# Kernel tuning notes

Measured on AMD Instinct MI355X. Metric: run time of the kernel, lower is better.

## Reference

```python
import jax, jax.numpy as jnp
import numpy as np


def rotary_pos_emb(x):
    # x: [..., seq, dim], dim even. Interleaved (GPT-NeoX-style pairwise) rotary.
    dim, seq = x.shape[-1], x.shape[-2]
    ts = jnp.arange(0, dim, 2, dtype=jnp.float32)
    inv_freqs = 10000.0 ** (-ts / dim)
    grid = jnp.arange(seq, dtype=jnp.float32)[:, None] * inv_freqs[None, :]  # [s, dim//2]
    sin = jnp.repeat(jnp.sin(grid), 2, axis=-1).astype(x.dtype)  # [s, dim]
    cos = jnp.repeat(jnp.cos(grid), 2, axis=-1).astype(x.dtype)  # [s, dim]
    x1, x2 = x[..., ::2], x[..., 1::2]
    xs = jnp.stack([-x2, x1], axis=-1).reshape(x.shape)  # interleave (-x2, x1)
    return x * cos + xs * sin


def setup_inputs() -> dict:
    key = jax.random.key(0)
    kx, kq, kk, kv, ko = jax.random.split(key, 5)
    B, S, D = 2, 2048, 1024
    scale = 1.0 / np.sqrt(D)
    x = jax.random.normal(kx, (B, S, D), dtype=jnp.float32)
    mask = jnp.tril(jnp.ones((S, S), dtype=bool))  # causal
    Wq = jax.random.normal(kq, (D, D), dtype=jnp.float32) * scale
    Wk = jax.random.normal(kk, (D, D), dtype=jnp.float32) * scale
    Wv = jax.random.normal(kv, (D, D), dtype=jnp.float32) * scale
    Wo = jax.random.normal(ko, (D, D), dtype=jnp.float32) * scale
    return {"x": x, "mask": mask, "Wq": Wq, "Wk": Wk, "Wv": Wv, "Wo": Wo}


def reference(x, mask, Wq, Wk, Wv, Wo):
    H = 16
    POS_PORTION = 0.5
    B, S, D = x.shape
    K = D // H
    p = int(K * POS_PORTION)

    q = (x @ Wq) / (K ** 0.5)
    q = q.reshape(B, S, H, K).transpose(0, 2, 1, 3)  # b h l k
    q = jnp.concatenate([rotary_pos_emb(q[..., :p]), q[..., p:]], axis=-1)

    k = (x @ Wk).reshape(B, S, H, K).transpose(0, 2, 1, 3)
    k = jnp.concatenate([rotary_pos_emb(k[..., :p]), k[..., p:]], axis=-1)

    v = (x @ Wv).reshape(B, S, H, K).transpose(0, 2, 1, 3)

    logits = jnp.einsum('bhik,bhjk->bhij', q, k)
    # full-precision masked softmax
    l32 = logits.astype(jnp.float32)
    l32 = jnp.where(mask, l32, -1e30)
    a = jax.nn.softmax(l32, axis=-1).astype(logits.dtype)

    y = jnp.einsum('bhij,bhjv->bhiv', a, v)
    y = y.transpose(0, 2, 1, 3).reshape(B, S, D)  # b l (h v)
    return y @ Wo
```

## Files before the change

### kernel.cpp

```cpp
#include <hip/hip_runtime.h>
#include <cstdint>
#include <cstddef>

typedef __bf16 bf16;
typedef __bf16 bf16x8 __attribute__((ext_vector_type(8)));
typedef float  f32x4  __attribute__((ext_vector_type(4)));
typedef short  s16x4  __attribute__((ext_vector_type(4)));

#define B_  2
#define S_  2048
#define D_  1024
#define H_  16
#define KH  64

__device__ __forceinline__ void gload_lds16(const bf16* gp, bf16* lds_base) {
    __builtin_amdgcn_global_load_lds(
        (const __attribute__((address_space(1))) unsigned int*)gp,
        (__attribute__((address_space(3))) unsigned int*)lds_base,
        16, 0, 0);
}

__global__ __launch_bounds__(256) void prep(
    const float* __restrict__ x, bf16* __restrict__ xb,
    const float* __restrict__ Wq, const float* __restrict__ Wk,
    const float* __restrict__ Wv, const float* __restrict__ Wo,
    bf16* __restrict__ WqkvT, bf16* __restrict__ WoT)
{
    __shared__ bf16 tl[64][72];
    int z = blockIdx.x;
    if (z < 4096) {
        const int i = (z * 256 + threadIdx.x) * 4;
        const float4 v = *(const float4*)(x + i);
        union { int2 w; bf16 e[4]; } u;
        u.e[0] = (bf16)v.x; u.e[1] = (bf16)v.y;
        u.e[2] = (bf16)v.z; u.e[3] = (bf16)v.w;
        *(int2*)(xb + i) = u.w;
        return;
    }
    z -= 4096;
    const int zx = z & 15, zy = (z >> 4) & 15, zw = z >> 8;
    const float* src = (zw == 0) ? Wq : (zw == 1) ? Wk : (zw == 2) ? Wv : Wo;
    bf16* dst = (zw < 3) ? (WqkvT + (size_t)zw * D_ * D_) : WoT;
    const int r0 = zy * 64;
    const int c0 = zx * 64;
    const int t  = threadIdx.x;
    {
        const int r = t >> 2, cs = (t & 3) * 16;
        const float4* p = (const float4*)(src + (size_t)(r0 + r) * D_ + c0 + cs);
        float4 a0 = p[0], a1 = p[1], a2 = p[2], a3 = p[3];
        tl[cs +  0][r] = (bf16)a0.x; tl[cs +  1][r] = (bf16)a0.y;
        tl[cs +  2][r] = (bf16)a0.z; tl[cs +  3][r] = (bf16)a0.w;
        tl[cs +  4][r] = (bf16)a1.x; tl[cs +  5][r] = (bf16)a1.y;
        tl[cs +  6][r] = (bf16)a1.z; tl[cs +  7][r] = (bf16)a1.w;
        tl[cs +  8][r] = (bf16)a2.x; tl[cs +  9][r] = (bf16)a2.y;
        tl[cs + 10][r] = (bf16)a2.z; tl[cs + 11][r] = (bf16)a2.w;
        tl[cs + 12][r] = (bf16)a3.x; tl[cs + 13][r] = (bf16)a3.y;
        tl[cs + 14][r] = (bf16)a3.z; tl[cs + 15][r] = (bf16)a3.w;
    }
    __syncthreads();
    {
        const int c = t >> 2, rs = (t & 3) * 16;
        union { int4 v[2]; bf16 e[16]; } u;
#pragma unroll
        for (int i = 0; i < 16; ++i) u.e[i] = tl[c][rs + i];
        int4* p = (int4*)(dst + (size_t)(c0 + c) * D_ + r0 + rs);
        p[0] = u.v[0]; p[1] = u.v[1];
    }
}

template <int EPI, int BN>
__global__ __launch_bounds__(256, 2) void gemm_bt(
    const bf16* __restrict__ A, const bf16* __restrict__ BT,
    float* __restrict__ C, int N, int Kd,
    bf16* __restrict__ qp, bf16* __restrict__ kp, bf16* __restrict__ vp)
{
    constexpr int NJF = BN / 32;
    __shared__ bf16 As[128 * 64];
    __shared__ bf16 Bs[BN * 64];
    const int tid  = threadIdx.x;
    const int lane = tid & 63;
    const int wave = tid >> 6;
    const int l15  = lane & 15;
    const int quad = lane >> 4;
    const int m0 = blockIdx.y * 128;
    const int n0 = blockIdx.x * BN;
    const int wm = (wave >> 1) * 64;
    const int wn = (wave & 1) * (BN / 2);

    f32x4 acc[4][NJF];
#pragma unroll
    for (int i = 0; i < 4; ++i)
#pragma unroll
        for (int j = 0; j < NJF; ++j) acc[i][j] = f32x4{0.f, 0.f, 0.f, 0.f};

    for (int k0 = 0; k0 < Kd; k0 += 64) {
        __syncthreads();
#pragma unroll
        for (int c = 0; c < 4; ++c) {
            const int base  = wave * 4096 + c * 1024;
            const int flatb = base + lane * 16;
            const int row   = flatb >> 7;
            const int col   = (flatb & 127) >> 1;
            gload_lds16(A + (size_t)(m0 + row) * Kd + k0 + col, As + (base >> 1));
        }
#pragma unroll
        for (int c = 0; c < NJF; ++c) {
            const int base  = wave * (BN * 32) + c * 1024;
            const int flatb = base + lane * 16;
            const int row   = flatb >> 7;
            const int col   = (flatb & 127) >> 1;
            gload_lds16(BT + (size_t)(n0 + row) * Kd + k0 + col, Bs + (base >> 1));
        }
        __syncthreads();
#pragma unroll
        for (int kk = 0; kk < 64; kk += 32) {
            bf16x8 af[4], bfv[NJF];
#pragma unroll
            for (int i = 0; i < 4; ++i)
                af[i] = *(const bf16x8*)&As[(wm + i * 16 + l15) * 64 + kk + quad * 8];
#pragma unroll
            for (int j = 0; j < NJF; ++j)
                bfv[j] = *(const bf16x8*)&Bs[(wn + j * 16 + l15) * 64 + kk + quad * 8];
#pragma unroll
            for (int i = 0; i < 4; ++i)
#pragma unroll
                for (int j = 0; j < NJF; ++j)
                    acc[i][j] = __builtin_amdgcn_mfma_f32_16x16x32_bf16(
                        af[i], bfv[j], acc[i][j], 0, 0, 0);
        }
    }

#pragma unroll
    for (int i = 0; i < 4; ++i)
#pragma unroll
        for (int j = 0; j < NJF; ++j) {
            const int Rb = m0 + wm + i * 16 + quad * 4;
            const int Cc = n0 + wn + j * 16 + l15;
            if (EPI == 0) {
#pragma unroll
                for (int r = 0; r < 4; ++r)
                    C[(size_t)(Rb + r) * N + Cc] = acc[i][j][r];
            } else {
                const int sec = Cc >> 10, cc = Cc & 1023;
                const int h = cc >> 6, kd = cc & 63;
#pragma unroll
                for (int r = 0; r < 4; ++r) {
                    const int row = Rb + r;
                    const int b = row >> 11, s = row & (S_ - 1);
                    float v = acc[i][j][r];
                    if (sec == 0) {
                        qp[((size_t)(b * H_ + h) * S_ + s) * KH + kd] =
                            (bf16)(v * 0.1803368801111204f);
                    } else if (sec == 1) {
                        if ((kd >> 4) < 2) {
                            const float partner = __shfl_xor(v, 1);
                            const float inv = __builtin_exp2f(
                                -(float)(kd >> 1) * (13.28771237954945f / 16.f));
                            const float ang = (float)s * inv;
                            float sn, cn;
                            __sincosf(ang, &sn, &cn);
                            v = (l15 & 1) ? fmaf(partner, sn, v * cn)
                                          : fmaf(-partner, sn, v * cn);
                        }
                        kp[((size_t)(b * H_ + h) * S_ + s) * KH + kd] = (bf16)v;
                    } else {
                        vp[((size_t)(b * H_ + h) * KH + kd) * S_ + s] = (bf16)v;
                    }
                }
            }
        }
}

__global__ __launch_bounds__(128, 2) void attn(
    const bf16* __restrict__ q, const bf16* __restrict__ k,
    const bf16* __restrict__ vt, bf16* __restrict__ y)
{
    __shared__ bf16 Ks[2][64 * 64];
    __shared__ bf16 VTs[2][64 * 64];

    const int z  = blockIdx.x;
    const int v_ = z & 7;
    const int u_ = (z >> 3) & 31;
    const int w_ = z >> 8;
    const int bh = u_;
    const int qt = (w_ == 0) ? v_ : (w_ == 1) ? (15 - v_)
                 : (w_ == 2) ? (16 + v_) : (31 - v_);
    const int b  = bh >> 4, h = bh & 15;
    const int t    = threadIdx.x;
    const int lane = t & 63, wave = t >> 6;
    const int l15  = lane & 15, quad = lane >> 4;
    const int wrow = qt * 64 + wave * 32;

    const bf16* kbh = k  + (size_t)bh * S_ * KH;
    const bf16* vbh = vt + (size_t)bh * KH * S_;

    const int srow = lane >> 3;
    const int sg   = (lane & 7) ^ srow;

    auto stage = [&](int jt, int bb) {
        const int j0 = jt * 64;
#pragma unroll
        for (int i = 0; i < 4; ++i) {
            const int c = wave * 4 + i;
            gload_lds16(kbh + (size_t)(j0 + c * 8 + srow) * KH + sg * 8,
                        &Ks[bb][c * 8 * 64]);
            gload_lds16(vbh + (size_t)(c * 8 + srow) * S_ + j0 + sg * 8,
                        &VTs[bb][c * 8 * 64]);
        }
    };

    bf16x8 qf[2][2];
#pragma unroll
    for (int mi = 0; mi < 2; ++mi) {
        const bf16* qp = q + ((size_t)bh * S_ + wrow + mi * 16 + l15) * KH + quad * 8;
        qf[mi][0] = *(const bf16x8*)qp;
        qf[mi][1] = *(const bf16x8*)(qp + 32);
        const float s = (float)(wrow + mi * 16 + l15);
#pragma unroll
        for (int tt = 0; tt < 4; ++tt) {
            const int i = quad * 4 + tt;
            const float inv = exp2f(-(float)i * (13.28771237954945f / 16.f));
            const float ang = s * inv;
            const float sn = sinf(ang), cn = cosf(ang);
            const float x0 = (float)qf[mi][0][2 * tt], x1 = (float)qf[mi][0][2 * tt + 1];
            qf[mi][0][2 * tt]     = (bf16)(x0 * cn - x1 * sn);
            qf[mi][0][2 * tt + 1] = (bf16)(x1 * cn + x0 * sn);
        }
    }

    s16x4 ones4;
#pragma unroll
    for (int i = 0; i < 4; ++i) ones4[i] = (short)0x3F80;

    f32x4 accO[2][4], lacc[2];
#pragma unroll
    for (int mi = 0; mi < 2; ++mi) {
#pragma unroll
        for (int j = 0; j < 4; ++j) accO[mi][j] = f32x4{0.f, 0.f, 0.f, 0.f};
        lacc[mi] = f32x4{0.f, 0.f, 0.f, 0.f};
    }

    const int nj = qt + 1;
    stage(0, 0);
    for (int jt = 0; jt < nj; ++jt) {
        const int bb = jt & 1;
        __syncthreads();
        if (jt + 1 < nj) stage(jt + 1, bb ^ 1);

        f32x4 accS[2][4];
#pragma unroll
        for (int mi = 0; mi < 2; ++mi)
#pragma unroll
            for (int nb = 0; nb < 4; ++nb) accS[mi][nb] = f32x4{0.f, 0.f, 0.f, 0.f};
#pragma unroll
        for (int c = 0; c < 2; ++c) {
            bf16x8 kf[4];
#pragma unroll
            for (int nb = 0; nb < 4; ++nb)
                kf[nb] = *(const bf16x8*)
                    &Ks[bb][(nb * 16 + l15) * 64 + (((c * 4 + quad) ^ (l15 & 7)) * 8)];
            __builtin_amdgcn_s_setprio(1);
#pragma unroll
            for (int mi = 0; mi < 2; ++mi)
#pragma unroll
                for (int nb = 0; nb < 4; ++nb)
                    accS[mi][nb] = __builtin_amdgcn_mfma_f32_16x16x32_bf16(
                        kf[nb], qf[mi][c], accS[mi][nb], 0, 0, 0);
            __builtin_amdgcn_s_setprio(0);
        }

        if (jt == nj - 1) {
            const int j0 = jt * 64;
#pragma unroll
            for (int mi = 0; mi < 2; ++mi)
#pragma unroll
                for (int nb = 0; nb < 4; ++nb)
#pragma unroll
                    for (int r = 0; r < 4; ++r) {
                        const int qi = wrow + mi * 16 + l15;
                        const int ki = j0 + nb * 16 + quad * 4 + r;
                        if (ki > qi) accS[mi][nb][r] = -1e30f;
                    }
        }

        s16x4 pf[2][4];
#pragma unroll
        for (int mi = 0; mi < 2; ++mi)
#pragma unroll
            for (int nb = 0; nb < 4; ++nb) {
                union { bf16 hh[4]; s16x4 ss; } u;
#pragma unroll
                for (int r = 0; r < 4; ++r)
                    u.hh[r] = (bf16)__builtin_amdgcn_exp2f(accS[mi][nb][r]);
                pf[mi][nb] = u.ss;
            }

#pragma unroll
        for (int nb = 0; nb < 4; ++nb) {
            s16x4 vf[4];
#pragma unroll
            for (int vb = 0; vb < 4; ++vb)
                vf[vb] = *(const s16x4*)
                    &VTs[bb][(vb * 16 + l15) * 64 +
                             (((nb * 2 + (quad >> 1)) ^ (l15 & 7)) * 8) + (quad & 1) * 4];
            __builtin_amdgcn_s_setprio(1);
#pragma unroll
            for (int mi = 0; mi < 2; ++mi) {
#pragma unroll
                for (int vb = 0; vb < 4; ++vb)
                    accO[mi][vb] = __builtin_amdgcn_mfma_f32_16x16x16bf16_1k(
                        pf[mi][nb], vf[vb], accO[mi][vb], 0, 0, 0);
                lacc[mi] = __builtin_amdgcn_mfma_f32_16x16x16bf16_1k(
                    pf[mi][nb], ones4, lacc[mi], 0, 0, 0);
            }
            __builtin_amdgcn_s_setprio(0);
        }
    }

#pragma unroll
    for (int mi = 0; mi < 2; ++mi) {
        float rinv[4];
#pragma unroll
        for (int r = 0; r < 4; ++r) rinv[r] = 1.0f / lacc[mi][r];
#pragma unroll
        for (int vb = 0; vb < 4; ++vb)
#pragma unroll
            for (int r = 0; r < 4; ++r) {
                const int row = wrow + mi * 16 + quad * 4 + r;
                const int col = h * KH + vb * 16 + l15;
                y[((size_t)b * S_ + row) * D_ + col] = (bf16)(accO[mi][vb][r] * rinv[r]);
            }
    }
}

extern "C" void kernel_launch(void* const* d_in, const int* in_sizes, int n_in,
                              void* d_out, int out_size, void* d_ws, size_t ws_size,
                              hipStream_t stream)
{
    (void)in_sizes; (void)n_in; (void)out_size; (void)ws_size;
    const float* x  = (const float*)d_in[0];
    const float* Wq = (const float*)d_in[2];
    const float* Wk = (const float*)d_in[3];
    const float* Wv = (const float*)d_in[4];
    const float* Wo = (const float*)d_in[5];
    float* out = (float*)d_out;

    char* ws = (char*)d_ws;
    bf16* WqkvT = (bf16*)(ws + 0);
    bf16* WoT   = (bf16*)(ws + 6291456);
    bf16* xb    = (bf16*)(ws + 8388608);
    bf16* qw    = (bf16*)(ws + 16777216);
    bf16* kw    = (bf16*)(ws + 25165824);
    bf16* vtw   = (bf16*)(ws + 33554432);
    bf16* yw    = (bf16*)(ws + 41943040);

    hipLaunchKernelGGL(prep, dim3(5120), dim3(256), 0, stream,
                       x, xb, Wq, Wk, Wv, Wo, WqkvT, WoT);
    hipLaunchKernelGGL((gemm_bt<1, 128>), dim3(24, 32), dim3(256), 0, stream,
                       xb, WqkvT, (float*)nullptr, 3072, 1024, qw, kw, vtw);
    hipLaunchKernelGGL(attn, dim3(1024), dim3(128), 0, stream, qw, kw, vtw, yw);
    hipLaunchKernelGGL((gemm_bt<0, 64>), dim3(16, 32), dim3(256), 0, stream,
                       yw, WoT, out, 1024, 1024,
                       (bf16*)nullptr, (bf16*)nullptr, (bf16*)nullptr);
}
```

Baseline: 204.8 us.

## Split attention work across four waves and vectorize V-transpose stores

The attention kernel now runs 256 threads per block, with each of four waves owning 16 query rows instead of two waves owning 32. This halves per-wave registers and increases occupancy, but each wave reloads the K and V fragments from LDS for fewer MFMAs. The QKV GEMM epilogue also writes the transposed V section as one 4-element bf16 vector per lane instead of four scalar strided stores, cutting store instruction count.

Result: faster. 192.7 us (-5.9%).

```diff
diff --git a/kernel.cpp b/kernel.cpp
--- a/kernel.cpp
+++ b/kernel.cpp
@@ -143,35 +143,41 @@
             } else {
                 const int sec = Cc >> 10, cc = Cc & 1023;
                 const int h = cc >> 6, kd = cc & 63;
-#pragma unroll
-                for (int r = 0; r < 4; ++r) {
-                    const int row = Rb + r;
-                    const int b = row >> 11, s = row & (S_ - 1);
-                    float v = acc[i][j][r];
-                    if (sec == 0) {
-                        qp[((size_t)(b * H_ + h) * S_ + s) * KH + kd] =
-                            (bf16)(v * 0.1803368801111204f);
-                    } else if (sec == 1) {
-                        if ((kd >> 4) < 2) {
-                            const float partner = __shfl_xor(v, 1);
-                            const float inv = __builtin_exp2f(
-                                -(float)(kd >> 1) * (13.28771237954945f / 16.f));
-                            const float ang = (float)s * inv;
-                            float sn, cn;
-                            __sincosf(ang, &sn, &cn);
-                            v = (l15 & 1) ? fmaf(partner, sn, v * cn)
-                                          : fmaf(-partner, sn, v * cn);
+                if (sec == 2) {
+                    const int b = Rb >> 11, s0 = Rb & (S_ - 1);
+                    union { s16x4 sv; bf16 e[4]; } pv;
+#pragma unroll
+                    for (int r = 0; r < 4; ++r) pv.e[r] = (bf16)acc[i][j][r];
+                    *(s16x4*)&vp[((size_t)(b * H_ + h) * KH + kd) * S_ + s0] = pv.sv;
+                } else {
+#pragma unroll
+                    for (int r = 0; r < 4; ++r) {
+                        const int row = Rb + r;
+                        const int b = row >> 11, s = row & (S_ - 1);
+                        float v = acc[i][j][r];
+                        if (sec == 0) {
+                            qp[((size_t)(b * H_ + h) * S_ + s) * KH + kd] =
+                                (bf16)(v * 0.1803368801111204f);
+                        } else {
+                            if ((kd >> 4) < 2) {
+                                const float partner = __shfl_xor(v, 1);
+                                const float inv = __builtin_exp2f(
+                                    -(float)(kd >> 1) * (13.28771237954945f / 16.f));
+                                const float ang = (float)s * inv;
+                                float sn, cn;
+                                __sincosf(ang, &sn, &cn);
+                                v = (l15 & 1) ? fmaf(partner, sn, v * cn)
+                                              : fmaf(-partner, sn, v * cn);
+                            }
+                            kp[((size_t)(b * H_ + h) * S_ + s) * KH + kd] = (bf16)v;
                         }
-                        kp[((size_t)(b * H_ + h) * S_ + s) * KH + kd] = (bf16)v;
-                    } else {
-                        vp[((size_t)(b * H_ + h) * KH + kd) * S_ + s] = (bf16)v;
                     }
                 }
             }
         }
 }
 
-__global__ __launch_bounds__(128, 2) void attn(
+__global__ __launch_bounds__(256, 4) void attn(
     const bf16* __restrict__ q, const bf16* __restrict__ k,
     const bf16* __restrict__ vt, bf16* __restrict__ y)
 {
@@ -189,7 +195,7 @@
     const int t    = threadIdx.x;
     const int lane = t & 63, wave = t >> 6;
     const int l15  = lane & 15, quad = lane >> 4;
-    const int wrow = qt * 64 + wave * 32;
+    const int wrow = qt * 64 + wave * 16;
 
     const bf16* kbh = k  + (size_t)bh * S_ * KH;
     const bf16* vbh = vt + (size_t)bh * KH * S_;
@@ -200,8 +206,8 @@
     auto stage = [&](int jt, int bb) {
         const int j0 = jt * 64;
 #pragma unroll
-        for (int i = 0; i < 4; ++i) {
-            const int c = wave * 4 + i;
+        for (int i = 0; i < 2; ++i) {
+            const int c = wave * 2 + i;
             gload_lds16(kbh + (size_t)(j0 + c * 8 + srow) * KH + sg * 8,
                         &Ks[bb][c * 8 * 64]);
             gload_lds16(vbh + (size_t)(c * 8 + srow) * S_ + j0 + sg * 8,
@@ -209,22 +215,21 @@
         }
     };
 
-    bf16x8 qf[2][2];
-#pragma unroll
-    for (int mi = 0; mi < 2; ++mi) {
-        const bf16* qp = q + ((size_t)bh * S_ + wrow + mi * 16 + l15) * KH + quad * 8;
-        qf[mi][0] = *(const bf16x8*)qp;
-        qf[mi][1] = *(const bf16x8*)(qp + 32);
-        const float s = (float)(wrow + mi * 16 + l15);
+    bf16x8 qf[2];
+    {
+        const bf16* qp = q + ((size_t)bh * S_ + wrow + l15) * KH + quad * 8;
+        qf[0] = *(const bf16x8*)qp;
+        qf[1] = *(const bf16x8*)(qp + 32);
+        const float s = (float)(wrow + l15);
 #pragma unroll
         for (int tt = 0; tt < 4; ++tt) {
             const int i = quad * 4 + tt;
             const float inv = exp2f(-(float)i * (13.28771237954945f / 16.f));
             const float ang = s * inv;
             const float sn = sinf(ang), cn = cosf(ang);
-            const float x0 = (float)qf[mi][0][2 * tt], x1 = (float)qf[mi][0][2 * tt + 1];
-            qf[mi][0][2 * tt]     = (bf16)(x0 * cn - x1 * sn);
-            qf[mi][0][2 * tt + 1] = (bf16)(x1 * cn + x0 * sn);
+            const float x0 = (float)qf[0][2 * tt], x1 = (float)qf[0][2 * tt + 1];
+            qf[0][2 * tt]     = (bf16)(x0 * cn - x1 * sn);
+            qf[0][2 * tt + 1] = (bf16)(x1 * cn + x0 * sn);
         }
     }
 
@@ -232,13 +237,10 @@
 #pragma unroll
     for (int i = 0; i < 4; ++i) ones4[i] = (short)0x3F80;
 
-    f32x4 accO[2][4], lacc[2];
-#pragma unroll
-    for (int mi = 0; mi < 2; ++mi) {
-#pragma unroll
-        for (int j = 0; j < 4; ++j) accO[mi][j] = f32x4{0.f, 0.f, 0.f, 0.f};
-        lacc[mi] = f32x4{0.f, 0.f, 0.f, 0.f};
-    }
+    f32x4 accO[4], lacc;
+#pragma unroll
+    for (int j = 0; j < 4; ++j) accO[j] = f32x4{0.f, 0.f, 0.f, 0.f};
+    lacc = f32x4{0.f, 0.f, 0.f, 0.f};
 
     const int nj = qt + 1;
     stage(0, 0);
@@ -247,11 +249,9 @@
         __syncthreads();
         if (jt + 1 < nj) stage(jt + 1, bb ^ 1);
 
-        f32x4 accS[2][4];
-#pragma unroll
-        for (int mi = 0; mi < 2; ++mi)
-#pragma unroll
-            for (int nb = 0; nb < 4; ++nb) accS[mi][nb] = f32x4{0.f, 0.f, 0.f, 0.f};
+        f32x4 accS[4];
+#pragma unroll
+        for (int nb = 0; nb < 4; ++nb) accS[nb] = f32x4{0.f, 0.f, 0.f, 0.f};
 #pragma unroll
         for (int c = 0; c < 2; ++c) {
             bf16x8 kf[4];
@@ -261,39 +261,33 @@
                     &Ks[bb][(nb * 16 + l15) * 64 + (((c * 4 + quad) ^ (l15 & 7)) * 8)];
             __builtin_amdgcn_s_setprio(1);
 #pragma unroll
-            for (int mi = 0; mi < 2; ++mi)
-#pragma unroll
-                for (int nb = 0; nb < 4; ++nb)
-                    accS[mi][nb] = __builtin_amdgcn_mfma_f32_16x16x32_bf16(
-                        kf[nb], qf[mi][c], accS[mi][nb], 0, 0, 0);
+            for (int nb = 0; nb < 4; ++nb)
+                accS[nb] = __builtin_amdgcn_mfma_f32_16x16x32_bf16(
+                    kf[nb], qf[c], accS[nb], 0, 0, 0);
             __builtin_amdgcn_s_setprio(0);
         }
 
         if (jt == nj - 1) {
             const int j0 = jt * 64;
-#pragma unroll
-            for (int mi = 0; mi < 2; ++mi)
-#pragma unroll
-                for (int nb = 0; nb < 4; ++nb)
-#pragma unroll
-                    for (int r = 0; r < 4; ++r) {
-                        const int qi = wrow + mi * 16 + l15;
-                        const int ki = j0 + nb * 16 + quad * 4 + r;
-                        if (ki > qi) accS[mi][nb][r] = -1e30f;
-                    }
-        }
-
-        s16x4 pf[2][4];
-#pragma unroll
-        for (int mi = 0; mi < 2; ++mi)
-#pragma unroll
-            for (int nb = 0; nb < 4; ++nb) {
-                union { bf16 hh[4]; s16x4 ss; } u;
-#pragma unroll
-                for (int r = 0; r < 4; ++r)
-                    u.hh[r] = (bf16)__builtin_amdgcn_exp2f(accS[mi][nb][r]);
-                pf[mi][nb] = u.ss;
-            }
+            const int qi = wrow + l15;
+#pragma unroll
+            for (int nb = 0; nb < 4; ++nb)
+#pragma unroll
+                for (int r = 0; r < 4; ++r) {
+                    const int ki = j0 + nb * 16 + quad * 4 + r;
+                    if (ki > qi) accS[nb][r] = -1e30f;
+                }
+        }
+
+        s16x4 pf[4];
+#pragma unroll
+        for (int nb = 0; nb < 4; ++nb) {
+            union { bf16 hh[4]; s16x4 ss; } u;
+#pragma unroll
+            for (int r = 0; r < 4; ++r)
+                u.hh[r] = (bf16)__builtin_amdgcn_exp2f(accS[nb][r]);
+            pf[nb] = u.ss;
+        }
 
 #pragma unroll
         for (int nb = 0; nb < 4; ++nb) {
@@ -305,32 +299,26 @@
                              (((nb * 2 + (quad >> 1)) ^ (l15 & 7)) * 8) + (quad & 1) * 4];
             __builtin_amdgcn_s_setprio(1);
 #pragma unroll
-            for (int mi = 0; mi < 2; ++mi) {
-#pragma unroll
-                for (int vb = 0; vb < 4; ++vb)
-                    accO[mi][vb] = __builtin_amdgcn_mfma_f32_16x16x16bf16_1k(
-                        pf[mi][nb], vf[vb], accO[mi][vb], 0, 0, 0);
-                lacc[mi] = __builtin_amdgcn_mfma_f32_16x16x16bf16_1k(
-                    pf[mi][nb], ones4, lacc[mi], 0, 0, 0);
-            }
+            for (int vb = 0; vb < 4; ++vb)
+                accO[vb] = __builtin_amdgcn_mfma_f32_16x16x16bf16_1k(
+                    pf[nb], vf[vb], accO[vb], 0, 0, 0);
+            lacc = __builtin_amdgcn_mfma_f32_16x16x16bf16_1k(
+                pf[nb], ones4, lacc, 0, 0, 0);
             __builtin_amdgcn_s_setprio(0);
         }
     }
 
-#pragma unroll
-    for (int mi = 0; mi < 2; ++mi) {
-        float rinv[4];
-#pragma unroll
-        for (int r = 0; r < 4; ++r) rinv[r] = 1.0f / lacc[mi][r];
-#pragma unroll
-        for (int vb = 0; vb < 4; ++vb)
-#pragma unroll
-            for (int r = 0; r < 4; ++r) {
-                const int row = wrow + mi * 16 + quad * 4 + r;
-                const int col = h * KH + vb * 16 + l15;
-                y[((size_t)b * S_ + row) * D_ + col] = (bf16)(accO[mi][vb][r] * rinv[r]);
-            }
-    }
+    float rinv[4];
+#pragma unroll
+    for (int r = 0; r < 4; ++r) rinv[r] = 1.0f / lacc[r];
+#pragma unroll
+    for (int vb = 0; vb < 4; ++vb)
+#pragma unroll
+        for (int r = 0; r < 4; ++r) {
+            const int row = wrow + quad * 4 + r;
+            const int col = h * KH + vb * 16 + l15;
+            y[((size_t)b * S_ + row) * D_ + col] = (bf16)(accO[vb][r] * rinv[r]);
+        }
 }
 
 extern "C" void kernel_launch(void* const* d_in, const int* in_sizes, int n_in,
@@ -358,7 +346,7 @@
                        x, xb, Wq, Wk, Wv, Wo, WqkvT, WoT);
     hipLaunchKernelGGL((gemm_bt<1, 128>), dim3(24, 32), dim3(256), 0, stream,
                        xb, WqkvT, (float*)nullptr, 3072, 1024, qw, kw, vtw);
-    hipLaunchKernelGGL(attn, dim3(1024), dim3(128), 0, stream, qw, kw, vtw, yw);
+    hipLaunchKernelGGL(attn, dim3(1024), dim3(256), 0, stream, qw, kw, vtw, yw);
     hipLaunchKernelGGL((gemm_bt<0, 64>), dim3(16, 32), dim3(256), 0, stream,
                        yw, WoT, out, 1024, 1024,
                        (bf16*)nullptr, (bf16*)nullptr, (bf16*)nullptr);
```
